# Kernel tuning notes

Measured on AMD Instinct MI355X. Metric: run time of the kernel, lower is better.

Reference implementation:

```python
import jax, jax.numpy as jnp
import numpy as np
import math

B, S, E, H, D = 2, 2048, 1024, 16, 64  # batch, seq, embed, heads, head_dim


def setup_inputs() -> dict:
    key = jax.random.key(0)
    ks = jax.random.split(key, 10)
    scale = 1.0 / math.sqrt(D)
    return {
        "query": jax.random.normal(ks[0], (B, S, E), jnp.float32),
        "key": jax.random.normal(ks[1], (B, S, E), jnp.float32),
        "value": jax.random.normal(ks[2], (B, S, E), jnp.float32),
        "mask": jax.random.randint(ks[3], (1, 1, S, S), 0, 2, jnp.int32),
        # nn.Linear(single_dim, single_dim) weights (out,in) and biases
        "Wq": jax.random.uniform(ks[4], (D, D), jnp.float32, -scale, scale),
        "bq": jax.random.uniform(ks[5], (D,), jnp.float32, -scale, scale),
        "Wk": jax.random.uniform(ks[6], (D, D), jnp.float32, -scale, scale),
        "bk": jax.random.uniform(ks[7], (D,), jnp.float32, -scale, scale),
        "Wv": jax.random.uniform(ks[8], (D, D), jnp.float32, -scale, scale),
        "bv": jax.random.uniform(ks[9], (D,), jnp.float32, -scale, scale),
    }


def reference(query, key, value, mask, Wq, bq, Wk, bk, Wv, bv):
    b, sq, _ = query.shape
    sk = key.shape[1]
    # (b, s, E) -> (b, H, s, D)
    q = query.reshape(b, sq, H, D).transpose(0, 2, 1, 3)
    k = key.reshape(b, sk, H, D).transpose(0, 2, 1, 3)
    v = value.reshape(b, sk, H, D).transpose(0, 2, 1, 3)
    # per-head shared Linear on last dim: x @ W^T + b
    q = jnp.einsum('bhsd,ed->bhse', q, Wq) + bq
    k = jnp.einsum('bhsd,ed->bhse', k, Wk) + bk
    v = jnp.einsum('bhsd,ed->bhse', v, Wv) + bv
    scores = jnp.einsum('bhqd,bhkd->bhqk', q, k) / math.sqrt(D)
    scores = jnp.where(mask == 0, jnp.float32(-1e20), scores)
    attn = jax.nn.softmax(scores, axis=-1)
    out = jnp.einsum('bhqk,bhkd->bhqd', attn, v)
    return out.transpose(0, 2, 1, 3).reshape(b, sq, H * D)
```

## Files before the change

### kernel.cpp

```cpp
#include <hip/hip_runtime.h>

#define S_LEN 2048
#define E_DIM 1024
#define NH 16
#define HD 64
#define NT (S_LEN / 64)
#define SCALE_L2E 0.18033688011112042f

typedef __bf16 bf16;
typedef __attribute__((ext_vector_type(4))) bf16 bf16x4;
typedef __attribute__((ext_vector_type(8))) bf16 bf16x8;
typedef __attribute__((ext_vector_type(4))) float f32x4;
typedef unsigned long long u64;
typedef unsigned int u32;

#define MFMA(a, b, c) __builtin_amdgcn_mfma_f32_16x16x32_bf16((a), (b), (c), 0, 0, 0)

__device__ __forceinline__ bf16x8 cvt8(f32x4 a, f32x4 b) {
  bf16x8 r;
  r[0] = (bf16)a[0]; r[1] = (bf16)a[1]; r[2] = (bf16)a[2]; r[3] = (bf16)a[3];
  r[4] = (bf16)b[0]; r[5] = (bf16)b[1]; r[6] = (bf16)b[2]; r[7] = (bf16)b[3];
  return r;
}

__device__ __forceinline__ bf16x8 load_cvt_frag(const float* p) {
  f32x4 a = *(const f32x4*)(p);
  f32x4 b = *(const f32x4*)(p + 16);
  return cvt8(a, b);
}

__global__ __launch_bounds__(256) void kvproj_k(
    const float* __restrict__ Kin, const float* __restrict__ Vin,
    const float* __restrict__ Wk, const float* __restrict__ bk,
    const float* __restrict__ Wv, const float* __restrict__ bv,
    const int* __restrict__ mask,
    bf16* __restrict__ KpF, bf16* __restrict__ VpF, u64* __restrict__ bits) {
  const int xcd = blockIdx.x & 7;
  const int idx = blockIdx.x >> 3;
  const int bh = xcd * 4 + (idx >> 5);
  const int sblk = idx & 31;
  const int h = bh & (NH - 1);
  const int b = bh >> 4;
  const int lane = threadIdx.x & 63;
  const int wave = threadIdx.x >> 6;
  const int g = lane >> 4;
  const int c16 = lane & 15;
  const int sbase = sblk * 64 + wave * 16;
  const int srow = sbase + c16;

  const float* xk = Kin + ((size_t)b * S_LEN + srow) * E_DIM + h * HD;
  const float* xv = Vin + ((size_t)b * S_LEN + srow) * E_DIM + h * HD;
  bf16x8 xkf[2], xvf[2];
#pragma unroll
  for (int c = 0; c < 2; ++c) {
    xkf[c] = load_cvt_frag(xk + 32 * c + 4 * g);
    xvf[c] = load_cvt_frag(xv + 32 * c + 4 * g);
  }

#pragma unroll
  for (int nt = 0; nt < 4; ++nt) {
    const float* wr = Wk + (16 * nt + c16) * HD + 4 * g;
    f32x4 acc = {0.f, 0.f, 0.f, 0.f};
    acc = MFMA(xkf[0], load_cvt_frag(wr), acc);
    acc = MFMA(xkf[1], load_cvt_frag(wr + 32), acc);
    const float bias = bk[16 * nt + c16];
    const size_t fidx = (((size_t)bh * 32 + sblk) * 4 + wave) * 2 + (nt >> 1);
    const int e = (c16 & 3) + 4 * (nt & 1);
#pragma unroll
    for (int r = 0; r < 4; ++r) {
      const int lane_p = (c16 >> 2) * 16 + 4 * g + r;
      KpF[fidx * 512 + lane_p * 8 + e] = (bf16)(acc[r] + bias);
    }
  }
#pragma unroll
  for (int nt = 0; nt < 4; ++nt) {
    const float* wr = Wv + (16 * nt + c16) * HD + 4 * g;
    f32x4 acc = {0.f, 0.f, 0.f, 0.f};
    acc = MFMA(load_cvt_frag(wr), xvf[0], acc);
    acc = MFMA(load_cvt_frag(wr + 32), xvf[1], acc);
    const size_t fidx = (((size_t)bh * 32 + sblk) * 4 + nt) * 2 + (wave >> 1);
    const int e = (c16 & 3) + 4 * (wave & 1);
#pragma unroll
    for (int r = 0; r < 4; ++r) {
      const int dout = 16 * nt + 4 * g + r;
      const int lane_p = (c16 >> 2) * 16 + 4 * g + r;
      VpF[fidx * 512 + lane_p * 8 + e] = (bf16)(acc[r] + bv[dout]);
    }
  }

  const int wbase = blockIdx.x * 64 + wave * 16;
  int mv[16];
#pragma unroll
  for (int i = 0; i < 16; ++i) mv[i] = mask[(size_t)(wbase + i) * 64 + lane];
#pragma unroll
  for (int i = 0; i < 16; ++i) {
    const u64 bb = __ballot(mv[i] != 0);
    const int w = wbase + i;
    if (lane == 0) bits[(size_t)(w & 31) * S_LEN + (w >> 5)] = bb;
  }
}

__global__ __launch_bounds__(512) void attn_k(
    const float* __restrict__ Qin, const float* __restrict__ Wq, const float* __restrict__ bq,
    const bf16* __restrict__ KpF, const bf16* __restrict__ VpF,
    const u64* __restrict__ mbits, float* __restrict__ out) {
  const int xcd = blockIdx.x & 7;
  const int idx = blockIdx.x >> 3;
  const int bh = xcd * 4 + (idx >> 4);
  const int qc = idx & 15;
  const int h = bh & (NH - 1);
  const int b = bh >> 4;
  const int lane = threadIdx.x & 63;
  const int wave = threadIdx.x >> 6;
  const int g = lane >> 4;
  const int c16 = lane & 15;
  const int qrow = qc * 128 + wave * 16 + c16;

  __shared__ __align__(16) bf16 lds_kv[2][16 * 512];

  const float* xq = Qin + ((size_t)b * S_LEN + qrow) * E_DIM + h * HD;
  bf16x8 xqf[2];
#pragma unroll
  for (int c = 0; c < 2; ++c) xqf[c] = load_cvt_frag(xq + 32 * c + 4 * g);
  f32x4 qt[4];
#pragma unroll
  for (int t = 0; t < 4; ++t) {
    const float* wr = Wq + (16 * t + c16) * HD + 4 * g;
    f32x4 acc = {0.f, 0.f, 0.f, 0.f};
    acc = MFMA(load_cvt_frag(wr), xqf[0], acc);
    acc = MFMA(load_cvt_frag(wr + 32), xqf[1], acc);
#pragma unroll
    for (int r = 0; r < 4; ++r) acc[r] = (acc[r] + bq[16 * t + 4 * g + r]) * SCALE_L2E;
    qt[t] = acc;
  }
  bf16x8 qfrag0 = cvt8(qt[0], qt[1]);
  bf16x8 qfrag1 = cvt8(qt[2], qt[3]);

  bf16x8 ones;
#pragma unroll
  for (int i = 0; i < 8; ++i) ones[i] = (bf16)1.0f;

  const bf16* ktile = KpF + ((size_t)bh * 32) * 4096;
  const bf16* vtile = VpF + ((size_t)bh * 32) * 4096;
  const u64* mrowT = mbits + qrow;

  f32x4 o[4] = {};
  f32x4 o5 = {};

#define STAGE(BUF, T)                                                              \
  {                                                                                \
    const bf16* ks_ = ktile + (size_t)(T) * 4096 + wave * 512 + lane * 8;          \
    const bf16* vs_ = vtile + (size_t)(T) * 4096 + wave * 512 + lane * 8;          \
    __builtin_amdgcn_global_load_lds(                                              \
        (const __attribute__((address_space(1))) u32*)ks_,                         \
        (__attribute__((address_space(3))) u32*)((BUF) + wave * 512), 16, 0, 0);   \
    __builtin_amdgcn_global_load_lds(                                              \
        (const __attribute__((address_space(1))) u32*)vs_,                         \
        (__attribute__((address_space(3))) u32*)((BUF) + 4096 + wave * 512), 16, 0, 0); \
  }

  bf16* const B0 = &lds_kv[0][0];
  bf16* const B1 = &lds_kv[1][0];

  u64 mca, mcb;

  STAGE(B0, 0)
  mca = mrowT[0];
  asm volatile("s_waitcnt vmcnt(1)" ::: "memory");
  asm volatile("s_barrier" ::: "memory");

#define ITER(BUF, NXT, MWC, MWN, T)                                               \
  {                                                                               \
    const bool more_ = (T) + 1 < NT;                                              \
    if (more_) {                                                                  \
      STAGE(NXT, (T) + 1)                                                         \
      MWN = mrowT[(size_t)((T) + 1) * S_LEN];                                     \
    }                                                                             \
    const u64 mw_ = MWC;                                                          \
    bf16x8 kf[8], vfr[8];                                                         \
    _Pragma("unroll") for (int f = 0; f < 8; ++f)                                 \
        kf[f] = *(const bf16x8*)((BUF) + f * 512 + lane * 8);                     \
    f32x4 st[4];                                                                  \
    __builtin_amdgcn_s_setprio(1);                                                \
    _Pragma("unroll") for (int ks = 0; ks < 4; ++ks) {                            \
      f32x4 acc = {0.f, 0.f, 0.f, 0.f};                                           \
      acc = MFMA(kf[2 * ks], qfrag0, acc);                                        \
      acc = MFMA(kf[2 * ks + 1], qfrag1, acc);                                    \
      st[ks] = acc;                                                               \
    }                                                                             \
    __builtin_amdgcn_s_setprio(0);                                                \
    _Pragma("unroll") for (int f = 0; f < 8; ++f)                                 \
        vfr[f] = *(const bf16x8*)((BUF) + 4096 + f * 512 + lane * 8);             \
    const u64 mws = mw_ >> (4 * g);                                               \
    const u32 mlo = (u32)mws;                                                     \
    const u32 mhi = (u32)(mws >> 32);                                             \
    _Pragma("unroll") for (int ks = 0; ks < 4; ++ks) {                            \
      const u32 mword = (ks < 2) ? mlo : mhi;                                     \
      const int base = (ks & 1) * 16;                                             \
      _Pragma("unroll") for (int r = 0; r < 4; ++r) {                             \
        const float p = __builtin_amdgcn_exp2f(st[ks][r]);                        \
        const int keep = __builtin_amdgcn_sbfe(mword, base + r, 1);               \
        st[ks][r] = __uint_as_float(__float_as_uint(p) & (u32)keep);              \
      }                                                                           \
    }                                                                             \
    const bf16x8 pfrag0 = cvt8(st[0], st[1]);                                     \
    const bf16x8 pfrag1 = cvt8(st[2], st[3]);                                     \
    __builtin_amdgcn_s_setprio(1);                                                \
    _Pragma("unroll") for (int t = 0; t < 4; ++t) {                               \
      o[t] = MFMA(vfr[2 * t], pfrag0, o[t]);                                      \
      o[t] = MFMA(vfr[2 * t + 1], pfrag1, o[t]);                                  \
    }                                                                             \
    o5 = MFMA(ones, pfrag0, o5);                                                  \
    o5 = MFMA(ones, pfrag1, o5);                                                  \
    __builtin_amdgcn_s_setprio(0);                                                \
    if (more_) asm volatile("s_waitcnt vmcnt(1)" ::: "memory");                   \
    else       asm volatile("s_waitcnt vmcnt(0)" ::: "memory");                   \
    asm volatile("s_barrier" ::: "memory");                                       \
  }

  for (int t = 0; t < NT; t += 2) {
    ITER(B0, B1, mca, mcb, t)
    ITER(B1, B0, mcb, mca, t + 1)
  }
#undef ITER
#undef STAGE

  const float inv = 1.0f / o5[0];
  float* orow = out + ((size_t)b * S_LEN + qrow) * E_DIM + h * HD;
#pragma unroll
  for (int t = 0; t < 4; ++t) {
    f32x4 v;
#pragma unroll
    for (int r = 0; r < 4; ++r) v[r] = o[t][r] * inv;
    *(f32x4*)(orow + 16 * t + 4 * g) = v;
  }
}

extern "C" void kernel_launch(void* const* d_in, const int* in_sizes, int n_in,
                              void* d_out, int out_size, void* d_ws, size_t ws_size,
                              hipStream_t stream) {
  const float* Q = (const float*)d_in[0];
  const float* K = (const float*)d_in[1];
  const float* V = (const float*)d_in[2];
  const int* mask = (const int*)d_in[3];
  const float* Wq = (const float*)d_in[4];
  const float* bq = (const float*)d_in[5];
  const float* Wk = (const float*)d_in[6];
  const float* bk = (const float*)d_in[7];
  const float* Wv = (const float*)d_in[8];
  const float* bv = (const float*)d_in[9];
  float* out = (float*)d_out;

  char* ws = (char*)d_ws;
  const size_t proj_bytes = (size_t)2 * NH * S_LEN * HD * 2;
  bf16* KpF = (bf16*)ws;
  bf16* VpF = (bf16*)(ws + proj_bytes);
  u64* mbits = (u64*)(ws + 2 * proj_bytes);

  kvproj_k<<<2 * NH * (S_LEN / 64), 256, 0, stream>>>(K, V, Wk, bk, Wv, bv, mask,
                                                      KpF, VpF, mbits);
  attn_k<<<2 * NH * (S_LEN / 128), 512, 0, stream>>>(Q, Wq, bq, KpF, VpF, mbits, out);
}
```

Baseline: 87.25 us.

## Quad-buffer K/V tiles two per barrier; stage projections in LDS for coalesced stores

The attention loop moves from double buffering with one barrier per 64-key tile to four LDS buffers. It prefetches two tiles ahead and computes two tiles per barrier phase, which halves barrier count and keeps more loads in flight. The K/V projection kernel now writes its bf16 fragments into shared memory first, then stores them to global memory as 16-byte vectors instead of scattered 2-byte writes. In exchange, the attention kernel's LDS use doubles to 64KB per block, which may limit how many blocks fit on a CU. The projection kernel also gains a block-wide barrier.

```diff
diff --git a/kernel.cpp b/kernel.cpp
--- a/kernel.cpp
+++ b/kernel.cpp
@@ -48,6 +48,9 @@
   const int sbase = sblk * 64 + wave * 16;
   const int srow = sbase + c16;
 
+  __shared__ __align__(16) bf16 lkb[4][2][512];
+  __shared__ __align__(16) bf16 lvb[8][512];
+
   const float* xk = Kin + ((size_t)b * S_LEN + srow) * E_DIM + h * HD;
   const float* xv = Vin + ((size_t)b * S_LEN + srow) * E_DIM + h * HD;
   bf16x8 xkf[2], xvf[2];
@@ -64,12 +67,11 @@
     acc = MFMA(xkf[0], load_cvt_frag(wr), acc);
     acc = MFMA(xkf[1], load_cvt_frag(wr + 32), acc);
     const float bias = bk[16 * nt + c16];
-    const size_t fidx = (((size_t)bh * 32 + sblk) * 4 + wave) * 2 + (nt >> 1);
     const int e = (c16 & 3) + 4 * (nt & 1);
 #pragma unroll
     for (int r = 0; r < 4; ++r) {
       const int lane_p = (c16 >> 2) * 16 + 4 * g + r;
-      KpF[fidx * 512 + lane_p * 8 + e] = (bf16)(acc[r] + bias);
+      lkb[wave][nt >> 1][lane_p * 8 + e] = (bf16)(acc[r] + bias);
     }
   }
 #pragma unroll
@@ -78,14 +80,27 @@
     f32x4 acc = {0.f, 0.f, 0.f, 0.f};
     acc = MFMA(load_cvt_frag(wr), xvf[0], acc);
     acc = MFMA(load_cvt_frag(wr + 32), xvf[1], acc);
-    const size_t fidx = (((size_t)bh * 32 + sblk) * 4 + nt) * 2 + (wave >> 1);
     const int e = (c16 & 3) + 4 * (wave & 1);
 #pragma unroll
     for (int r = 0; r < 4; ++r) {
       const int dout = 16 * nt + 4 * g + r;
       const int lane_p = (c16 >> 2) * 16 + 4 * g + r;
-      VpF[fidx * 512 + lane_p * 8 + e] = (bf16)(acc[r] + bv[dout]);
+      lvb[nt * 2 + (wave >> 1)][lane_p * 8 + e] = (bf16)(acc[r] + bv[dout]);
     }
+  }
+  __syncthreads();
+
+  const size_t base = ((size_t)bh * 32 + sblk) * 4;
+#pragma unroll
+  for (int c = 0; c < 2; ++c) {
+    const bf16x8 v = *(const bf16x8*)&lkb[wave][c][lane * 8];
+    *(bf16x8*)(KpF + ((base + wave) * 2 + c) * 512 + lane * 8) = v;
+  }
+#pragma unroll
+  for (int i = 0; i < 2; ++i) {
+    const int fi = 2 * wave + i;
+    const bf16x8 v = *(const bf16x8*)&lvb[fi][lane * 8];
+    *(bf16x8*)(VpF + ((base + (fi >> 1)) * 2 + (fi & 1)) * 512 + lane * 8) = v;
   }
 
   const int wbase = blockIdx.x * 64 + wave * 16;
@@ -116,7 +131,7 @@
   const int c16 = lane & 15;
   const int qrow = qc * 128 + wave * 16 + c16;
 
-  __shared__ __align__(16) bf16 lds_kv[2][16 * 512];
+  __shared__ __align__(16) bf16 lds_kv[4][16 * 512];
 
   const float* xq = Qin + ((size_t)b * S_LEN + qrow) * E_DIM + h * HD;
   bf16x8 xqf[2];
@@ -159,24 +174,8 @@
         (__attribute__((address_space(3))) u32*)((BUF) + 4096 + wave * 512), 16, 0, 0); \
   }
 
-  bf16* const B0 = &lds_kv[0][0];
-  bf16* const B1 = &lds_kv[1][0];
-
-  u64 mca, mcb;
-
-  STAGE(B0, 0)
-  mca = mrowT[0];
-  asm volatile("s_waitcnt vmcnt(1)" ::: "memory");
-  asm volatile("s_barrier" ::: "memory");
-
-#define ITER(BUF, NXT, MWC, MWN, T)                                               \
+#define COMPUTE(BUF, MW)                                                          \
   {                                                                               \
-    const bool more_ = (T) + 1 < NT;                                              \
-    if (more_) {                                                                  \
-      STAGE(NXT, (T) + 1)                                                         \
-      MWN = mrowT[(size_t)((T) + 1) * S_LEN];                                     \
-    }                                                                             \
-    const u64 mw_ = MWC;                                                          \
     bf16x8 kf[8], vfr[8];                                                         \
     _Pragma("unroll") for (int f = 0; f < 8; ++f)                                 \
         kf[f] = *(const bf16x8*)((BUF) + f * 512 + lane * 8);                     \
@@ -191,7 +190,7 @@
     __builtin_amdgcn_s_setprio(0);                                                \
     _Pragma("unroll") for (int f = 0; f < 8; ++f)                                 \
         vfr[f] = *(const bf16x8*)((BUF) + 4096 + f * 512 + lane * 8);             \
-    const u64 mws = mw_ >> (4 * g);                                               \
+    const u64 mws = (MW) >> (4 * g);                                              \
     const u32 mlo = (u32)mws;                                                     \
     const u32 mhi = (u32)(mws >> 32);                                             \
     _Pragma("unroll") for (int ks = 0; ks < 4; ++ks) {                            \
@@ -213,16 +212,43 @@
     o5 = MFMA(ones, pfrag0, o5);                                                  \
     o5 = MFMA(ones, pfrag1, o5);                                                  \
     __builtin_amdgcn_s_setprio(0);                                                \
-    if (more_) asm volatile("s_waitcnt vmcnt(1)" ::: "memory");                   \
-    else       asm volatile("s_waitcnt vmcnt(0)" ::: "memory");                   \
+  }
+
+  bf16* const B0 = &lds_kv[0][0];
+  bf16* const B1 = &lds_kv[1][0];
+  bf16* const B2 = &lds_kv[2][0];
+  bf16* const B3 = &lds_kv[3][0];
+
+  u64 mA, mB, mC, mD;
+
+  STAGE(B0, 0)
+  STAGE(B1, 1)
+  mA = mrowT[0];
+  mB = mrowT[S_LEN];
+  asm volatile("s_waitcnt vmcnt(2)" ::: "memory");
+  asm volatile("s_barrier" ::: "memory");
+
+#define PHASE(BA, BB, SA, SB, MC0, MC1, MN0, MN1, T)                              \
+  {                                                                               \
+    const bool m2_ = (T) + 2 < NT;                                                \
+    const bool m3_ = (T) + 3 < NT;                                                \
+    if (m2_) STAGE(SA, (T) + 2)                                                   \
+    if (m3_) STAGE(SB, (T) + 3)                                                   \
+    if (m2_) MN0 = mrowT[(size_t)((T) + 2) * S_LEN];                              \
+    if (m3_) MN1 = mrowT[(size_t)((T) + 3) * S_LEN];                              \
+    COMPUTE(BA, MC0)                                                              \
+    COMPUTE(BB, MC1)                                                              \
+    if (m2_) asm volatile("s_waitcnt vmcnt(2)" ::: "memory");                     \
+    else     asm volatile("s_waitcnt vmcnt(0)" ::: "memory");                     \
     asm volatile("s_barrier" ::: "memory");                                       \
   }
 
-  for (int t = 0; t < NT; t += 2) {
-    ITER(B0, B1, mca, mcb, t)
-    ITER(B1, B0, mcb, mca, t + 1)
-  }
-#undef ITER
+  for (int t = 0; t < NT; t += 4) {
+    PHASE(B0, B1, B2, B3, mA, mB, mC, mD, t)
+    PHASE(B2, B3, B0, B1, mC, mD, mA, mB, t + 2)
+  }
+#undef PHASE
+#undef COMPUTE
 #undef STAGE
 
   const float inv = 1.0f / o5[0];
```

After: 80.44 us, median of 2. 1.08x faster.

## Coalesce K/V projection stores through LDS and halve attention block size

Applied to the files above, without the earlier changes.

The K/V projection kernel now writes its scattered bf16 fragment values into shared memory first. After a barrier it copies them out to global memory with 16-byte vector stores, instead of issuing strided 2-byte global stores. The attention kernel goes from 512 threads covering 128 query rows to 256 threads covering 64 rows, which doubles the number of blocks. Each wave now stages two K and two V fragments per tile so the four waves still load the whole tile. This gives better CU occupancy and load balance, at the cost of each K/V tile being fetched by twice as many blocks.

```diff
diff --git a/kernel.cpp b/kernel.cpp
--- a/kernel.cpp
+++ b/kernel.cpp
@@ -48,6 +48,9 @@
   const int sbase = sblk * 64 + wave * 16;
   const int srow = sbase + c16;
 
+  __shared__ __align__(16) bf16 lkb[4][2][512];
+  __shared__ __align__(16) bf16 lvb[8][512];
+
   const float* xk = Kin + ((size_t)b * S_LEN + srow) * E_DIM + h * HD;
   const float* xv = Vin + ((size_t)b * S_LEN + srow) * E_DIM + h * HD;
   bf16x8 xkf[2], xvf[2];
@@ -64,12 +67,11 @@
     acc = MFMA(xkf[0], load_cvt_frag(wr), acc);
     acc = MFMA(xkf[1], load_cvt_frag(wr + 32), acc);
     const float bias = bk[16 * nt + c16];
-    const size_t fidx = (((size_t)bh * 32 + sblk) * 4 + wave) * 2 + (nt >> 1);
     const int e = (c16 & 3) + 4 * (nt & 1);
 #pragma unroll
     for (int r = 0; r < 4; ++r) {
       const int lane_p = (c16 >> 2) * 16 + 4 * g + r;
-      KpF[fidx * 512 + lane_p * 8 + e] = (bf16)(acc[r] + bias);
+      lkb[wave][nt >> 1][lane_p * 8 + e] = (bf16)(acc[r] + bias);
     }
   }
 #pragma unroll
@@ -78,14 +80,27 @@
     f32x4 acc = {0.f, 0.f, 0.f, 0.f};
     acc = MFMA(load_cvt_frag(wr), xvf[0], acc);
     acc = MFMA(load_cvt_frag(wr + 32), xvf[1], acc);
-    const size_t fidx = (((size_t)bh * 32 + sblk) * 4 + nt) * 2 + (wave >> 1);
     const int e = (c16 & 3) + 4 * (wave & 1);
 #pragma unroll
     for (int r = 0; r < 4; ++r) {
       const int dout = 16 * nt + 4 * g + r;
       const int lane_p = (c16 >> 2) * 16 + 4 * g + r;
-      VpF[fidx * 512 + lane_p * 8 + e] = (bf16)(acc[r] + bv[dout]);
+      lvb[nt * 2 + (wave >> 1)][lane_p * 8 + e] = (bf16)(acc[r] + bv[dout]);
     }
+  }
+  __syncthreads();
+
+  const size_t base = ((size_t)bh * 32 + sblk) * 4;
+#pragma unroll
+  for (int c = 0; c < 2; ++c) {
+    const bf16x8 v = *(const bf16x8*)&lkb[wave][c][lane * 8];
+    *(bf16x8*)(KpF + ((base + wave) * 2 + c) * 512 + lane * 8) = v;
+  }
+#pragma unroll
+  for (int i = 0; i < 2; ++i) {
+    const int fi = 2 * wave + i;
+    const bf16x8 v = *(const bf16x8*)&lvb[fi][lane * 8];
+    *(bf16x8*)(VpF + ((base + (fi >> 1)) * 2 + (fi & 1)) * 512 + lane * 8) = v;
   }
 
   const int wbase = blockIdx.x * 64 + wave * 16;
@@ -100,21 +115,21 @@
   }
 }
 
-__global__ __launch_bounds__(512) void attn_k(
+__global__ __launch_bounds__(256) void attn_k(
     const float* __restrict__ Qin, const float* __restrict__ Wq, const float* __restrict__ bq,
     const bf16* __restrict__ KpF, const bf16* __restrict__ VpF,
     const u64* __restrict__ mbits, float* __restrict__ out) {
   const int xcd = blockIdx.x & 7;
   const int idx = blockIdx.x >> 3;
-  const int bh = xcd * 4 + (idx >> 4);
-  const int qc = idx & 15;
+  const int bh = xcd * 4 + (idx >> 5);
+  const int qc = idx & 31;
   const int h = bh & (NH - 1);
   const int b = bh >> 4;
   const int lane = threadIdx.x & 63;
   const int wave = threadIdx.x >> 6;
   const int g = lane >> 4;
   const int c16 = lane & 15;
-  const int qrow = qc * 128 + wave * 16 + c16;
+  const int qrow = qc * 64 + wave * 16 + c16;
 
   __shared__ __align__(16) bf16 lds_kv[2][16 * 512];
 
@@ -149,14 +164,20 @@
 
 #define STAGE(BUF, T)                                                              \
   {                                                                                \
-    const bf16* ks_ = ktile + (size_t)(T) * 4096 + wave * 512 + lane * 8;          \
-    const bf16* vs_ = vtile + (size_t)(T) * 4096 + wave * 512 + lane * 8;          \
+    const bf16* ks_ = ktile + (size_t)(T) * 4096 + (2 * wave) * 512 + lane * 8;    \
+    const bf16* vs_ = vtile + (size_t)(T) * 4096 + (2 * wave) * 512 + lane * 8;    \
     __builtin_amdgcn_global_load_lds(                                              \
         (const __attribute__((address_space(1))) u32*)ks_,                         \
-        (__attribute__((address_space(3))) u32*)((BUF) + wave * 512), 16, 0, 0);   \
+        (__attribute__((address_space(3))) u32*)((BUF) + (2 * wave) * 512), 16, 0, 0); \
+    __builtin_amdgcn_global_load_lds(                                              \
+        (const __attribute__((address_space(1))) u32*)(ks_ + 512),                 \
+        (__attribute__((address_space(3))) u32*)((BUF) + (2 * wave + 1) * 512), 16, 0, 0); \
     __builtin_amdgcn_global_load_lds(                                              \
         (const __attribute__((address_space(1))) u32*)vs_,                         \
-        (__attribute__((address_space(3))) u32*)((BUF) + 4096 + wave * 512), 16, 0, 0); \
+        (__attribute__((address_space(3))) u32*)((BUF) + 4096 + (2 * wave) * 512), 16, 0, 0); \
+    __builtin_amdgcn_global_load_lds(                                              \
+        (const __attribute__((address_space(1))) u32*)(vs_ + 512),                 \
+        (__attribute__((address_space(3))) u32*)((BUF) + 4096 + (2 * wave + 1) * 512), 16, 0, 0); \
   }
 
   bf16* const B0 = &lds_kv[0][0];
@@ -259,5 +280,5 @@
 
   kvproj_k<<<2 * NH * (S_LEN / 64), 256, 0, stream>>>(K, V, Wk, bk, Wv, bv, mask,
                                                       KpF, VpF, mbits);
-  attn_k<<<2 * NH * (S_LEN / 128), 512, 0, stream>>>(Q, Wq, bq, KpF, VpF, mbits, out);
-}
+  attn_k<<<2 * NH * (S_LEN / 64), 256, 0, stream>>>(Q, Wq, bq, KpF, VpF, mbits, out);
+}
```

Result: slower. 90.61 us (+3.8%).
